# Optimization experiments

Measured on AMD Instinct MI355X. Metric: run time of the kernel, lower is better.

The kernel has to match this reference:

```python
import jax, jax.numpy as jnp
import numpy as np

N = 50000   # nodes
E = 800000  # edges
F = 128     # feature dim per layer
BN_EPS = 1e-5


def setup_inputs() -> dict:
    key = jax.random.key(0)
    ks = jax.random.split(key, 4)
    x = jax.random.normal(ks[0], (N, F), dtype=jnp.float32)
    edge_index = jax.random.randint(ks[1], (2, E), 0, N, dtype=jnp.int64)
    scale = 1.0 / np.sqrt(F)
    W1 = jax.random.normal(ks[2], (F, F), dtype=jnp.float32) * scale
    W2 = jax.random.normal(ks[3], (F, F), dtype=jnp.float32) * scale
    zeros = jnp.zeros((F,), dtype=jnp.float32)
    ones = jnp.ones((F,), dtype=jnp.float32)
    prelu = jnp.full((1,), 0.25, dtype=jnp.float32)
    return {
        "x": x, "edge_index": edge_index,
        "W1": W1, "b1": zeros, "g1": ones, "be1": zeros, "a1": prelu,
        "W2": W2, "b2": zeros, "g2": ones, "be2": zeros, "a2": prelu,
    }


def _gcn_norm(edge_index):
    # PyG GCNConv: add self-loops, symmetric normalization D^-1/2 A D^-1/2
    src, dst = edge_index[0], edge_index[1]
    loop = jnp.arange(N, dtype=src.dtype)
    src_a = jnp.concatenate([src, loop])  # [E+N]
    dst_a = jnp.concatenate([dst, loop])
    w = jnp.ones((E + N,), dtype=jnp.float32)
    deg = jax.ops.segment_sum(w, dst_a, num_segments=N)
    dinv = jnp.where(deg > 0, jax.lax.rsqrt(jnp.maximum(deg, 1.0)), 0.0)
    norm = dinv[src_a] * w * dinv[dst_a]  # [E+N]
    return src_a, dst_a, norm


def _layer(x, src_a, dst_a, norm, W, b, g, be, a):
    h = x @ W                                    # [N,F] dense transform
    msg = h[src_a] * norm[:, None]               # gather [E+N,F]
    agg = jax.ops.segment_sum(msg, dst_a, num_segments=N) + b  # scatter-add
    # BatchNorm1d (training mode: biased batch statistics over nodes)
    mu = jnp.mean(agg, axis=0)
    var = jnp.mean(jnp.square(agg - mu), axis=0)
    xh = (agg - mu) * jax.lax.rsqrt(var + BN_EPS) * g + be
    # PReLU (single shared weight)
    return jnp.where(xh >= 0, xh, a * xh)


def reference(x, edge_index, W1, b1, g1, be1, a1, W2, b2, g2, be2, a2):
    src_a, dst_a, norm = _gcn_norm(edge_index)
    x = _layer(x, src_a, dst_a, norm, W1, b1, g1, be1, a1)
    x = _layer(x, src_a, dst_a, norm, W2, b2, g2, be2, a2)
    return x
```

## Files before the change

### kernel.cpp

```cpp
#include <hip/hip_runtime.h>

#define FD 128
#define BN_EPS 1e-5f
#define BSH 8
#define CAP 6144
#define BE 8192
#define NGB 2048
#define NRB 64

typedef short s8v __attribute__((ext_vector_type(8)));
typedef float f4v __attribute__((ext_vector_type(4)));

__device__ __forceinline__ unsigned short f2bf(float f) {
    unsigned u = __float_as_uint(f);
    u += 0x7fff + ((u >> 16) & 1);
    return (unsigned short)(u >> 16);
}
__device__ __forceinline__ unsigned pack2(float a, float b) {
    return (unsigned)f2bf(a) | ((unsigned)f2bf(b) << 16);
}
__device__ __forceinline__ float bf_lo(unsigned int u) {
    return __uint_as_float(u << 16);
}
__device__ __forceinline__ float bf_hi(unsigned int u) {
    return __uint_as_float(u & 0xffff0000u);
}
__device__ __forceinline__ float bfu(unsigned short s) {
    return __uint_as_float(((unsigned)s) << 16);
}

__device__ __forceinline__ int edge_get(const void* ei, int is64, size_t idx) {
    return is64 ? (int)((const long long*)ei)[idx] : ((const int*)ei)[idx];
}

__global__ __launch_bounds__(256) void partition_kernel(const void* ei,
                                                        int* __restrict__ gcur,
                                                        unsigned* __restrict__ slab, int E) {
    __shared__ int any;
    __shared__ int hist[256];
    __shared__ int base[256];
    __shared__ int cur[256];
    int t = threadIdx.x;
    if (t == 0) any = 0;
    hist[t] = 0;
    __syncthreads();
    {
        const int* e32 = (const int*)ei;
        int limit = 2 * E < 4096 ? 2 * E : 4096;
        int found = 0;
        for (int i = t * 2 + 1; i < limit; i += 512)
            if (e32[i] != 0) { found = 1; break; }
        if (found) atomicOr(&any, 1);
    }
    __syncthreads();
    int is64 = any ? 0 : 1;
    int e0 = blockIdx.x * BE;
    int cnt = E - e0; if (cnt > BE) cnt = BE;
    for (int i = t; i < cnt; i += 256) {
        int d = edge_get(ei, is64, (size_t)E + e0 + i);
        atomicAdd(&hist[d >> BSH], 1);
    }
    __syncthreads();
    base[t] = hist[t] ? atomicAdd(&gcur[t], hist[t]) : 0;
    cur[t] = 0;
    __syncthreads();
    for (int i = t; i < cnt; i += 256) {
        int s = edge_get(ei, is64, e0 + i);
        int d = edge_get(ei, is64, (size_t)E + e0 + i);
        int b = d >> BSH;
        int r = atomicAdd(&cur[b], 1);
        int pos = base[b] + r;
        if (pos < CAP)
            slab[(size_t)b * CAP + pos] = (unsigned)s | ((unsigned)(d & 255) << 24);
    }
}

__global__ __launch_bounds__(256) void bucket_csr_kernel(const unsigned* __restrict__ slab,
                                                         const int* __restrict__ gcur,
                                                         int* __restrict__ colslab,
                                                         uint4* __restrict__ nodemeta,
                                                         float* __restrict__ dinv, int n) {
    __shared__ int hist[256];
    __shared__ int loc[256];
    __shared__ int cur[256];
    __shared__ int tmp[256];
    int b = blockIdx.x, t = threadIdx.x;
    hist[t] = 0;
    __syncthreads();
    int cnt = gcur[b]; if (cnt > CAP) cnt = CAP;
    const unsigned* sl = slab + (size_t)b * CAP;
    for (int i = t; i < cnt; i += 256)
        atomicAdd(&hist[sl[i] >> 24], 1);
    __syncthreads();
    int v = hist[t];
    tmp[t] = v;
    __syncthreads();
    for (int off = 1; off < 256; off <<= 1) {
        int x = (t >= off) ? tmp[t - off] : 0;
        __syncthreads();
        tmp[t] += x;
        __syncthreads();
    }
    int start_loc = tmp[t] - v;
    loc[t] = start_loc;
    cur[t] = 0;
    int node = (b << BSH) + t;
    if (node < n) {
        float dv = rsqrtf(1.0f + (float)v);
        dinv[node] = dv;
        nodemeta[node] = make_uint4((unsigned)(b * CAP + start_loc), (unsigned)v,
                                    __float_as_uint(dv), 0u);
    }
    __syncthreads();
    for (int i = t; i < cnt; i += 256) {
        unsigned e = sl[i];
        int dl = e >> 24;
        int r = atomicAdd(&cur[dl], 1);
        colslab[(size_t)b * CAP + loc[dl] + r] = (int)(e & 0xFFFFFF);
    }
}

__global__ __launch_bounds__(256) void wprep_kernel(const float* __restrict__ W1,
                                                    const float* __restrict__ W2,
                                                    unsigned short* __restrict__ Wf1,
                                                    unsigned short* __restrict__ Wf2) {
    int blk = blockIdx.x;
    const float* W = (blk < 64) ? W1 : W2;
    unsigned short* Wf = (blk < 64) ? Wf1 : Wf2;
    int idx = (blk & 63) * 256 + threadIdx.x;
    int j = idx & 7, lane = (idx >> 3) & 63, ct = (idx >> 9) & 7, kt = idx >> 12;
    int k = kt * 32 + (lane >> 4) * 8 + j;
    int c = ct * 16 + (lane & 15);
    Wf[idx] = f2bf(W[k * FD + c]);
}

template<int MODE>
__global__ __launch_bounds__(256) void gemm_mfma_kernel(const void* __restrict__ Ain,
                                                        const unsigned short* __restrict__ Wfrag,
                                                        const float* __restrict__ dinv,
                                                        const float4* __restrict__ scsh,
                                                        const float* __restrict__ aP,
                                                        unsigned short* __restrict__ C,
                                                        int n) {
    int wave = threadIdx.x >> 6, lane = threadIdx.x & 63;
    int rbase = blockIdx.x * 64 + wave * 16;
    int lrow = rbase + (lane & 15);
    int kg = lane >> 4;
    bool rok = lrow < n;
    float alpha = MODE ? aP[0] : 0.f;

    f4v acc[8];
#pragma unroll
    for (int i = 0; i < 8; ++i) acc[i] = (f4v){0.f, 0.f, 0.f, 0.f};

    const s8v* wf = (const s8v*)Wfrag;

#pragma unroll
    for (int kt = 0; kt < 4; ++kt) {
        s8v afr = (s8v){0, 0, 0, 0, 0, 0, 0, 0};
        if (rok) {
            float4 u0, u1;
            if (MODE) {
                const unsigned short* A = (const unsigned short*)Ain;
                s8v raw = *(const s8v*)(A + (size_t)lrow * FD + kt * 32 + kg * 8);
                u0.x = bfu((unsigned short)raw[0]); u0.y = bfu((unsigned short)raw[1]);
                u0.z = bfu((unsigned short)raw[2]); u0.w = bfu((unsigned short)raw[3]);
                u1.x = bfu((unsigned short)raw[4]); u1.y = bfu((unsigned short)raw[5]);
                u1.z = bfu((unsigned short)raw[6]); u1.w = bfu((unsigned short)raw[7]);
                int c4 = kt * 8 + kg * 2;
                float4 sc0 = scsh[c4],      sh0 = scsh[32 + c4];
                float4 sc1 = scsh[c4 + 1],  sh1 = scsh[32 + c4 + 1];
                u0.x = u0.x * sc0.x + sh0.x; u0.y = u0.y * sc0.y + sh0.y;
                u0.z = u0.z * sc0.z + sh0.z; u0.w = u0.w * sc0.w + sh0.w;
                u1.x = u1.x * sc1.x + sh1.x; u1.y = u1.y * sc1.y + sh1.y;
                u1.z = u1.z * sc1.z + sh1.z; u1.w = u1.w * sc1.w + sh1.w;
                u0.x = u0.x >= 0.f ? u0.x : alpha * u0.x;
                u0.y = u0.y >= 0.f ? u0.y : alpha * u0.y;
                u0.z = u0.z >= 0.f ? u0.z : alpha * u0.z;
                u0.w = u0.w >= 0.f ? u0.w : alpha * u0.w;
                u1.x = u1.x >= 0.f ? u1.x : alpha * u1.x;
                u1.y = u1.y >= 0.f ? u1.y : alpha * u1.y;
                u1.z = u1.z >= 0.f ? u1.z : alpha * u1.z;
                u1.w = u1.w >= 0.f ? u1.w : alpha * u1.w;
            } else {
                const float* A = (const float*)Ain;
                const float* p = A + (size_t)lrow * FD + kt * 32 + kg * 8;
                u0 = *(const float4*)p;
                u1 = *(const float4*)(p + 4);
            }
            afr[0] = (short)f2bf(u0.x); afr[1] = (short)f2bf(u0.y);
            afr[2] = (short)f2bf(u0.z); afr[3] = (short)f2bf(u0.w);
            afr[4] = (short)f2bf(u1.x); afr[5] = (short)f2bf(u1.y);
            afr[6] = (short)f2bf(u1.z); afr[7] = (short)f2bf(u1.w);
        }
#pragma unroll
        for (int ct = 0; ct < 8; ++ct) {
            s8v bfr = wf[(kt * 8 + ct) * 64 + lane];
            acc[ct] = __builtin_amdgcn_mfma_f32_16x16x32_bf16(afr, bfr, acc[ct], 0, 0, 0);
        }
    }

    int col0 = lane & 15;
#pragma unroll
    for (int r = 0; r < 4; ++r) {
        int row = rbase + kg * 4 + r;
        if (row < n) {
            float dv = dinv[row];
            unsigned short* crow = C + (size_t)row * FD;
#pragma unroll
            for (int ct = 0; ct < 8; ++ct)
                crow[ct * 16 + col0] = f2bf(acc[ct][r] * dv);
        }
    }
}

__global__ __launch_bounds__(256) void gather_stats_kernel(const uint2* __restrict__ hs2,
                                                           const uint4* __restrict__ nodemeta,
                                                           const int* __restrict__ col,
                                                           const float* __restrict__ b,
                                                           uint2* __restrict__ aggb,
                                                           float4* __restrict__ partial,
                                                           int n) {
    __shared__ float4 redS[256];
    __shared__ float4 redQ[256];
    int tid = threadIdx.x;
    int hid = blockIdx.x * 8 + (tid >> 5);
    int q = tid & 31;
    float4 bb = ((const float4*)b)[q];

    float4 ssum = {0.f, 0.f, 0.f, 0.f};
    float4 ssq  = {0.f, 0.f, 0.f, 0.f};

    for (int wid = hid; wid < n; wid += NGB * 8) {
        uint4 m = nodemeta[wid];
        int i0 = (int)m.x, cnt = (int)m.y;
        float dv = __uint_as_float(m.z);
        uint2 u = hs2[(size_t)wid * 32 + q];
        float ax = bf_lo(u.x), ay = bf_hi(u.x), az = bf_lo(u.y), aw = bf_hi(u.y);
        int j = 0;
        for (; j + 4 <= cnt; j += 4) {
            int s0 = col[i0 + j], s1 = col[i0 + j + 1];
            int s2 = col[i0 + j + 2], s3 = col[i0 + j + 3];
            uint2 u0 = hs2[(size_t)s0 * 32 + q];
            uint2 u1 = hs2[(size_t)s1 * 32 + q];
            uint2 u2 = hs2[(size_t)s2 * 32 + q];
            uint2 u3 = hs2[(size_t)s3 * 32 + q];
            ax += bf_lo(u0.x) + bf_lo(u1.x) + bf_lo(u2.x) + bf_lo(u3.x);
            ay += bf_hi(u0.x) + bf_hi(u1.x) + bf_hi(u2.x) + bf_hi(u3.x);
            az += bf_lo(u0.y) + bf_lo(u1.y) + bf_lo(u2.y) + bf_lo(u3.y);
            aw += bf_hi(u0.y) + bf_hi(u1.y) + bf_hi(u2.y) + bf_hi(u3.y);
        }
        for (; j < cnt; ++j) {
            int s = col[i0 + j];
            uint2 uu = hs2[(size_t)s * 32 + q];
            ax += bf_lo(uu.x); ay += bf_hi(uu.x); az += bf_lo(uu.y); aw += bf_hi(uu.y);
        }
        float4 o;
        o.x = dv * ax + bb.x; o.y = dv * ay + bb.y;
        o.z = dv * az + bb.z; o.w = dv * aw + bb.w;
        uint2 w;
        w.x = pack2(o.x, o.y);
        w.y = pack2(o.z, o.w);
        aggb[(size_t)wid * 32 + q] = w;
        ssum.x += o.x; ssum.y += o.y; ssum.z += o.z; ssum.w += o.w;
        ssq.x += o.x * o.x; ssq.y += o.y * o.y;
        ssq.z += o.z * o.z; ssq.w += o.w * o.w;
    }
    redS[tid] = ssum;
    redQ[tid] = ssq;
    __syncthreads();
    if (tid < 128) {
        redS[tid].x += redS[tid+128].x; redS[tid].y += redS[tid+128].y;
        redS[tid].z += redS[tid+128].z; redS[tid].w += redS[tid+128].w;
        redQ[tid].x += redQ[tid+128].x; redQ[tid].y += redQ[tid+128].y;
        redQ[tid].z += redQ[tid+128].z; redQ[tid].w += redQ[tid+128].w;
    }
    __syncthreads();
    if (tid < 64) {
        redS[tid].x += redS[tid+64].x; redS[tid].y += redS[tid+64].y;
        redS[tid].z += redS[tid+64].z; redS[tid].w += redS[tid+64].w;
        redQ[tid].x += redQ[tid+64].x; redQ[tid].y += redQ[tid+64].y;
        redQ[tid].z += redQ[tid+64].z; redQ[tid].w += redQ[tid+64].w;
    }
    __syncthreads();
    if (tid < 32) {
        float4 s = redS[tid], s2 = redS[tid + 32];
        float4 qq = redQ[tid], q2 = redQ[tid + 32];
        s.x += s2.x; s.y += s2.y; s.z += s2.z; s.w += s2.w;
        qq.x += q2.x; qq.y += q2.y; qq.z += q2.z; qq.w += q2.w;
        partial[(size_t)blockIdx.x * 64 + tid] = s;
        partial[(size_t)blockIdx.x * 64 + 32 + tid] = qq;
    }
}

__global__ __launch_bounds__(256) void reduce_partial_kernel(const float4* __restrict__ partial,
                                                             float4* __restrict__ partial2) {
    __shared__ float4 red[256];
    int t = threadIdx.x;
    int e = t & 63;
    int sr = t >> 6;
    int r0 = blockIdx.x * 32;
    float4 acc = {0.f, 0.f, 0.f, 0.f};
    for (int r = sr; r < 32; r += 4) {
        float4 v = partial[(size_t)(r0 + r) * 64 + e];
        acc.x += v.x; acc.y += v.y; acc.z += v.z; acc.w += v.w;
    }
    red[t] = acc;
    __syncthreads();
    if (sr < 2) {
        float4 o = red[t + 128];
        red[t].x += o.x; red[t].y += o.y; red[t].z += o.z; red[t].w += o.w;
    }
    __syncthreads();
    if (sr == 0) {
        float4 o = red[t + 64];
        float4 s = red[t];
        s.x += o.x; s.y += o.y; s.z += o.z; s.w += o.w;
        partial2[(size_t)blockIdx.x * 64 + e] = s;
    }
}

__global__ __launch_bounds__(1024) void bn_finalize_kernel(const float4* __restrict__ partial2,
                                                           const float* __restrict__ g,
                                                           const float* __restrict__ be,
                                                           float4* __restrict__ scsh,
                                                           float invn) {
    __shared__ float4 red[1024];
    int t = threadIdx.x;
    int e = t & 63;
    int rg = t >> 6;
    float4 acc = {0.f, 0.f, 0.f, 0.f};
    for (int r = rg; r < NRB; r += 16) {
        float4 v = partial2[(size_t)r * 64 + e];
        acc.x += v.x; acc.y += v.y; acc.z += v.z; acc.w += v.w;
    }
    red[t] = acc;
    __syncthreads();
#pragma unroll
    for (int s = 8; s >= 1; s >>= 1) {
        if (rg < s) {
            float4 o = red[t + s * 64];
            red[t].x += o.x; red[t].y += o.y; red[t].z += o.z; red[t].w += o.w;
        }
        __syncthreads();
    }
    if (t < 32) {
        float4 s = red[t];
        float4 qq = red[32 + t];
        float4 gg = ((const float4*)g)[t];
        float4 bbe = ((const float4*)be)[t];
        float4 mu, var, sc, sh;
        mu.x = s.x * invn; mu.y = s.y * invn; mu.z = s.z * invn; mu.w = s.w * invn;
        var.x = qq.x * invn - mu.x * mu.x; var.y = qq.y * invn - mu.y * mu.y;
        var.z = qq.z * invn - mu.z * mu.z; var.w = qq.w * invn - mu.w * mu.w;
        sc.x = gg.x * rsqrtf(var.x + BN_EPS); sc.y = gg.y * rsqrtf(var.y + BN_EPS);
        sc.z = gg.z * rsqrtf(var.z + BN_EPS); sc.w = gg.w * rsqrtf(var.w + BN_EPS);
        sh.x = bbe.x - mu.x * sc.x; sh.y = bbe.y - mu.y * sc.y;
        sh.z = bbe.z - mu.z * sc.z; sh.w = bbe.w - mu.w * sc.w;
        scsh[t] = sc;
        scsh[32 + t] = sh;
    }
}

__global__ __launch_bounds__(256) void bn_apply_kernel(const uint2* __restrict__ aggb,
                                                       const float4* __restrict__ scsh,
                                                       const float* __restrict__ aP,
                                                       float4* __restrict__ out, int n) {
    int t = blockIdx.x * 256 + threadIdx.x;
    if (t >= n * 32) return;
    int c4 = t & 31;
    float alpha = aP[0];
    uint2 u = aggb[t];
    float4 v;
    v.x = bf_lo(u.x); v.y = bf_hi(u.x); v.z = bf_lo(u.y); v.w = bf_hi(u.y);
    float4 sc = scsh[c4];
    float4 sh = scsh[32 + c4];
    float4 y;
    y.x = v.x * sc.x + sh.x; y.y = v.y * sc.y + sh.y;
    y.z = v.z * sc.z + sh.z; y.w = v.w * sc.w + sh.w;
    y.x = y.x >= 0.f ? y.x : alpha * y.x;
    y.y = y.y >= 0.f ? y.y : alpha * y.y;
    y.z = y.z >= 0.f ? y.z : alpha * y.z;
    y.w = y.w >= 0.f ? y.w : alpha * y.w;
    out[t] = y;
}


extern "C" void kernel_launch(void* const* d_in, const int* in_sizes, int n_in,
                              void* d_out, int out_size, void* d_ws, size_t ws_size,
                              hipStream_t stream) {
    const float* x  = (const float*)d_in[0];
    const void*  ei = d_in[1];
    const float* W1 = (const float*)d_in[2];
    const float* b1 = (const float*)d_in[3];
    const float* g1 = (const float*)d_in[4];
    const float* be1= (const float*)d_in[5];
    const float* a1 = (const float*)d_in[6];
    const float* W2 = (const float*)d_in[7];
    const float* b2 = (const float*)d_in[8];
    const float* g2 = (const float*)d_in[9];
    const float* be2= (const float*)d_in[10];
    const float* a2 = (const float*)d_in[11];

    int N = in_sizes[0] / FD;
    int E = in_sizes[1] / 2;
    float* out = (float*)d_out;

    int nbuck = (N + (1 << BSH) - 1) >> BSH;

    char* ws = (char*)d_ws;
    size_t off = 0;
    auto alloc = [&](size_t bytes) {
        void* p = ws + off;
        off += (bytes + 255) & ~(size_t)255;
        return p;
    };
    float* dinv    = (float*)alloc((size_t)N * 4);
    int*   gcur    = (int*)alloc(256 * 4);
    uint4* nodemeta= (uint4*)alloc((size_t)N * 16);
    unsigned* slab = (unsigned*)alloc((size_t)nbuck * CAP * 4);
    int*   colslab = (int*)alloc((size_t)nbuck * CAP * 4);
    unsigned short* wf1 = (unsigned short*)alloc((size_t)FD * FD * 2);
    unsigned short* wf2 = (unsigned short*)alloc((size_t)FD * FD * 2);
    unsigned short* hs  = (unsigned short*)alloc((size_t)N * FD * 2);
    uint2* aggb    = (uint2*)alloc((size_t)N * FD * 2);
    float4* partial= (float4*)alloc((size_t)NGB * 64 * 16);
    float4* partial2=(float4*)alloc((size_t)NRB * 64 * 16);
    float4* scsh   = (float4*)alloc(64 * 16);
    (void)ws_size; (void)n_in; (void)out_size;

    hipMemsetAsync(gcur, 0, 256 * 4, stream);

    partition_kernel<<<(E + BE - 1) / BE, 256, 0, stream>>>(ei, gcur, slab, E);
    bucket_csr_kernel<<<nbuck, 256, 0, stream>>>(slab, gcur, colslab, nodemeta, dinv, N);

    wprep_kernel<<<128, 256, 0, stream>>>(W1, W2, wf1, wf2);

    int gemm_blocks = (N + 63) / 64;
    int nt = N * 32;
    float invn = 1.0f / (float)N;

    gemm_mfma_kernel<0><<<gemm_blocks, 256, 0, stream>>>(x, wf1, dinv, nullptr, nullptr,
                                                         hs, N);
    gather_stats_kernel<<<NGB, 256, 0, stream>>>((const uint2*)hs, nodemeta, colslab,
                                                 b1, aggb, partial, N);
    reduce_partial_kernel<<<NRB, 256, 0, stream>>>(partial, partial2);
    bn_finalize_kernel<<<1, 1024, 0, stream>>>(partial2, g1, be1, scsh, invn);

    gemm_mfma_kernel<1><<<gemm_blocks, 256, 0, stream>>>(aggb, wf2, dinv,
                                                         scsh, a1, hs, N);
    gather_stats_kernel<<<NGB, 256, 0, stream>>>((const uint2*)hs, nodemeta, colslab,
                                                 b2, aggb, partial, N);
    reduce_partial_kernel<<<NRB, 256, 0, stream>>>(partial, partial2);
    bn_finalize_kernel<<<1, 1024, 0, stream>>>(partial2, g2, be2, scsh, invn);
    bn_apply_kernel<<<(nt + 255) / 256, 256, 0, stream>>>(aggb, scsh, a2, (float4*)out, N);
}
```

Before: 165.2 us.

## Widen gather loads, fuse BN reduce and finalize, fold counter reset

The gather kernel now has each half-warp read 16-byte bf16 rows. Two lane groups split a node's edge list, and their partial sums are combined with a cross-lane shuffle. Stats partials are written as flat floats. The two-stage BN reduction and the finalize kernel become one kernel, where the last block to finish (found with an atomic counter) computes scale and shift. The memset for the partition counter is folded into the weight-prep kernel, which now launches first. Together these aim to cut kernel launches and issue wider, fewer memory requests in the edge gather. The cost is threadfence and atomic ordering, plus shuffles and lane divergence in the gather.

Result: slower. 181.5 us (+9.9%).

```diff
diff --git a/kernel.cpp b/kernel.cpp
--- a/kernel.cpp
+++ b/kernel.cpp
@@ -31,6 +31,22 @@
 
 __device__ __forceinline__ int edge_get(const void* ei, int is64, size_t idx) {
     return is64 ? (int)((const long long*)ei)[idx] : ((const int*)ei)[idx];
+}
+
+__global__ __launch_bounds__(256) void wprep_kernel(const float* __restrict__ W1,
+                                                    const float* __restrict__ W2,
+                                                    unsigned short* __restrict__ Wf1,
+                                                    unsigned short* __restrict__ Wf2,
+                                                    int* __restrict__ gcur) {
+    int blk = blockIdx.x;
+    if (blk == 0 && threadIdx.x < 258) gcur[threadIdx.x] = 0;
+    const float* W = (blk < 64) ? W1 : W2;
+    unsigned short* Wf = (blk < 64) ? Wf1 : Wf2;
+    int idx = (blk & 63) * 256 + threadIdx.x;
+    int j = idx & 7, lane = (idx >> 3) & 63, ct = (idx >> 9) & 7, kt = idx >> 12;
+    int k = kt * 32 + (lane >> 4) * 8 + j;
+    int c = ct * 16 + (lane & 15);
+    Wf[idx] = f2bf(W[k * FD + c]);
 }
 
 __global__ __launch_bounds__(256) void partition_kernel(const void* ei,
@@ -118,20 +134,6 @@
         int r = atomicAdd(&cur[dl], 1);
         colslab[(size_t)b * CAP + loc[dl] + r] = (int)(e & 0xFFFFFF);
     }
-}
-
-__global__ __launch_bounds__(256) void wprep_kernel(const float* __restrict__ W1,
-                                                    const float* __restrict__ W2,
-                                                    unsigned short* __restrict__ Wf1,
-                                                    unsigned short* __restrict__ Wf2) {
-    int blk = blockIdx.x;
-    const float* W = (blk < 64) ? W1 : W2;
-    unsigned short* Wf = (blk < 64) ? Wf1 : Wf2;
-    int idx = (blk & 63) * 256 + threadIdx.x;
-    int j = idx & 7, lane = (idx >> 3) & 63, ct = (idx >> 9) & 7, kt = idx >> 12;
-    int k = kt * 32 + (lane >> 4) * 8 + j;
-    int c = ct * 16 + (lane & 15);
-    Wf[idx] = f2bf(W[k * FD + c]);
 }
 
 template<int MODE>
@@ -214,97 +216,148 @@
     }
 }
 
-__global__ __launch_bounds__(256) void gather_stats_kernel(const uint2* __restrict__ hs2,
+__global__ __launch_bounds__(256) void gather_stats_kernel(const uint4* __restrict__ hs4,
                                                            const uint4* __restrict__ nodemeta,
                                                            const int* __restrict__ col,
                                                            const float* __restrict__ b,
-                                                           uint2* __restrict__ aggb,
-                                                           float4* __restrict__ partial,
+                                                           uint4* __restrict__ aggb4,
+                                                           float* __restrict__ partialf,
+                                                           int* __restrict__ done,
                                                            int n) {
-    __shared__ float4 redS[256];
-    __shared__ float4 redQ[256];
+    __shared__ float redS[1024];
+    __shared__ float redQ[1024];
     int tid = threadIdx.x;
-    int hid = blockIdx.x * 8 + (tid >> 5);
-    int q = tid & 31;
-    float4 bb = ((const float4*)b)[q];
-
-    float4 ssum = {0.f, 0.f, 0.f, 0.f};
-    float4 ssq  = {0.f, 0.f, 0.f, 0.f};
+    if (blockIdx.x == 0 && tid == 0) done[0] = 0;
+    int half = tid >> 5;
+    int g = (tid >> 4) & 1;
+    int c = tid & 15;
+    int hid = blockIdx.x * 8 + half;
+
+    float bb[8];
+    {
+        const float4* b4 = (const float4*)b;
+        float4 blo = b4[c * 2], bhi = b4[c * 2 + 1];
+        bb[0] = blo.x; bb[1] = blo.y; bb[2] = blo.z; bb[3] = blo.w;
+        bb[4] = bhi.x; bb[5] = bhi.y; bb[6] = bhi.z; bb[7] = bhi.w;
+    }
+    float ss[8], sq[8];
+#pragma unroll
+    for (int k = 0; k < 8; ++k) { ss[k] = 0.f; sq[k] = 0.f; }
 
     for (int wid = hid; wid < n; wid += NGB * 8) {
         uint4 m = nodemeta[wid];
         int i0 = (int)m.x, cnt = (int)m.y;
         float dv = __uint_as_float(m.z);
-        uint2 u = hs2[(size_t)wid * 32 + q];
-        float ax = bf_lo(u.x), ay = bf_hi(u.x), az = bf_lo(u.y), aw = bf_hi(u.y);
-        int j = 0;
-        for (; j + 4 <= cnt; j += 4) {
-            int s0 = col[i0 + j], s1 = col[i0 + j + 1];
-            int s2 = col[i0 + j + 2], s3 = col[i0 + j + 3];
-            uint2 u0 = hs2[(size_t)s0 * 32 + q];
-            uint2 u1 = hs2[(size_t)s1 * 32 + q];
-            uint2 u2 = hs2[(size_t)s2 * 32 + q];
-            uint2 u3 = hs2[(size_t)s3 * 32 + q];
-            ax += bf_lo(u0.x) + bf_lo(u1.x) + bf_lo(u2.x) + bf_lo(u3.x);
-            ay += bf_hi(u0.x) + bf_hi(u1.x) + bf_hi(u2.x) + bf_hi(u3.x);
-            az += bf_lo(u0.y) + bf_lo(u1.y) + bf_lo(u2.y) + bf_lo(u3.y);
-            aw += bf_hi(u0.y) + bf_hi(u1.y) + bf_hi(u2.y) + bf_hi(u3.y);
-        }
-        for (; j < cnt; ++j) {
+        float a[8];
+#pragma unroll
+        for (int k = 0; k < 8; ++k) a[k] = 0.f;
+        if (g == 0) {
+            uint4 u = hs4[(size_t)wid * 16 + c];
+            a[0] += bf_lo(u.x); a[1] += bf_hi(u.x); a[2] += bf_lo(u.y); a[3] += bf_hi(u.y);
+            a[4] += bf_lo(u.z); a[5] += bf_hi(u.z); a[6] += bf_lo(u.w); a[7] += bf_hi(u.w);
+        }
+        int j = g;
+        for (; j + 6 < cnt; j += 8) {
+            int s0 = col[i0 + j],     s1 = col[i0 + j + 2];
+            int s2 = col[i0 + j + 4], s3 = col[i0 + j + 6];
+            uint4 u0 = hs4[(size_t)s0 * 16 + c];
+            uint4 u1 = hs4[(size_t)s1 * 16 + c];
+            uint4 u2 = hs4[(size_t)s2 * 16 + c];
+            uint4 u3 = hs4[(size_t)s3 * 16 + c];
+            a[0] += bf_lo(u0.x) + bf_lo(u1.x) + bf_lo(u2.x) + bf_lo(u3.x);
+            a[1] += bf_hi(u0.x) + bf_hi(u1.x) + bf_hi(u2.x) + bf_hi(u3.x);
+            a[2] += bf_lo(u0.y) + bf_lo(u1.y) + bf_lo(u2.y) + bf_lo(u3.y);
+            a[3] += bf_hi(u0.y) + bf_hi(u1.y) + bf_hi(u2.y) + bf_hi(u3.y);
+            a[4] += bf_lo(u0.z) + bf_lo(u1.z) + bf_lo(u2.z) + bf_lo(u3.z);
+            a[5] += bf_hi(u0.z) + bf_hi(u1.z) + bf_hi(u2.z) + bf_hi(u3.z);
+            a[6] += bf_lo(u0.w) + bf_lo(u1.w) + bf_lo(u2.w) + bf_lo(u3.w);
+            a[7] += bf_hi(u0.w) + bf_hi(u1.w) + bf_hi(u2.w) + bf_hi(u3.w);
+        }
+        for (; j < cnt; j += 2) {
             int s = col[i0 + j];
-            uint2 uu = hs2[(size_t)s * 32 + q];
-            ax += bf_lo(uu.x); ay += bf_hi(uu.x); az += bf_lo(uu.y); aw += bf_hi(uu.y);
-        }
-        float4 o;
-        o.x = dv * ax + bb.x; o.y = dv * ay + bb.y;
-        o.z = dv * az + bb.z; o.w = dv * aw + bb.w;
-        uint2 w;
-        w.x = pack2(o.x, o.y);
-        w.y = pack2(o.z, o.w);
-        aggb[(size_t)wid * 32 + q] = w;
-        ssum.x += o.x; ssum.y += o.y; ssum.z += o.z; ssum.w += o.w;
-        ssq.x += o.x * o.x; ssq.y += o.y * o.y;
-        ssq.z += o.z * o.z; ssq.w += o.w * o.w;
-    }
-    redS[tid] = ssum;
-    redQ[tid] = ssq;
+            uint4 u = hs4[(size_t)s * 16 + c];
+            a[0] += bf_lo(u.x); a[1] += bf_hi(u.x); a[2] += bf_lo(u.y); a[3] += bf_hi(u.y);
+            a[4] += bf_lo(u.z); a[5] += bf_hi(u.z); a[6] += bf_lo(u.w); a[7] += bf_hi(u.w);
+        }
+#pragma unroll
+        for (int k = 0; k < 8; ++k) a[k] += __shfl_xor(a[k], 16);
+        if (g == 0) {
+            float o[8];
+#pragma unroll
+            for (int k = 0; k < 8; ++k) o[k] = dv * a[k] + bb[k];
+            uint4 w;
+            w.x = pack2(o[0], o[1]); w.y = pack2(o[2], o[3]);
+            w.z = pack2(o[4], o[5]); w.w = pack2(o[6], o[7]);
+            aggb4[(size_t)wid * 16 + c] = w;
+#pragma unroll
+            for (int k = 0; k < 8; ++k) { ss[k] += o[k]; sq[k] += o[k] * o[k]; }
+        }
+    }
+    if (g == 0) {
+#pragma unroll
+        for (int k = 0; k < 8; ++k) {
+            redS[half * 128 + c * 8 + k] = ss[k];
+            redQ[half * 128 + c * 8 + k] = sq[k];
+        }
+    }
     __syncthreads();
     if (tid < 128) {
-        redS[tid].x += redS[tid+128].x; redS[tid].y += redS[tid+128].y;
-        redS[tid].z += redS[tid+128].z; redS[tid].w += redS[tid+128].w;
-        redQ[tid].x += redQ[tid+128].x; redQ[tid].y += redQ[tid+128].y;
-        redQ[tid].z += redQ[tid+128].z; redQ[tid].w += redQ[tid+128].w;
-    }
-    __syncthreads();
-    if (tid < 64) {
-        redS[tid].x += redS[tid+64].x; redS[tid].y += redS[tid+64].y;
-        redS[tid].z += redS[tid+64].z; redS[tid].w += redS[tid+64].w;
-        redQ[tid].x += redQ[tid+64].x; redQ[tid].y += redQ[tid+64].y;
-        redQ[tid].z += redQ[tid+64].z; redQ[tid].w += redQ[tid+64].w;
-    }
-    __syncthreads();
-    if (tid < 32) {
-        float4 s = redS[tid], s2 = redS[tid + 32];
-        float4 qq = redQ[tid], q2 = redQ[tid + 32];
-        s.x += s2.x; s.y += s2.y; s.z += s2.z; s.w += s2.w;
-        qq.x += q2.x; qq.y += q2.y; qq.z += q2.z; qq.w += q2.w;
-        partial[(size_t)blockIdx.x * 64 + tid] = s;
-        partial[(size_t)blockIdx.x * 64 + 32 + tid] = qq;
-    }
-}
-
-__global__ __launch_bounds__(256) void reduce_partial_kernel(const float4* __restrict__ partial,
-                                                             float4* __restrict__ partial2) {
+        float s = 0.f, q = 0.f;
+#pragma unroll
+        for (int h = 0; h < 8; ++h) {
+            s += redS[h * 128 + tid];
+            q += redQ[h * 128 + tid];
+        }
+        partialf[(size_t)blockIdx.x * 256 + tid] = s;
+        partialf[(size_t)blockIdx.x * 256 + 128 + tid] = q;
+    }
+}
+
+__global__ __launch_bounds__(256) void reduce_finalize_kernel(const float4* __restrict__ partial,
+                                                              float4* __restrict__ partial2,
+                                                              int* __restrict__ done,
+                                                              const float* __restrict__ g,
+                                                              const float* __restrict__ be,
+                                                              float4* __restrict__ scsh,
+                                                              float invn) {
     __shared__ float4 red[256];
+    __shared__ int isLast;
     int t = threadIdx.x;
     int e = t & 63;
     int sr = t >> 6;
-    int r0 = blockIdx.x * 32;
+    {
+        int r0 = blockIdx.x * 32;
+        float4 acc = {0.f, 0.f, 0.f, 0.f};
+        for (int r = sr; r < 32; r += 4) {
+            float4 v = partial[(size_t)(r0 + r) * 64 + e];
+            acc.x += v.x; acc.y += v.y; acc.z += v.z; acc.w += v.w;
+        }
+        red[t] = acc;
+        __syncthreads();
+        if (sr < 2) {
+            float4 o = red[t + 128];
+            red[t].x += o.x; red[t].y += o.y; red[t].z += o.z; red[t].w += o.w;
+        }
+        __syncthreads();
+        if (sr == 0) {
+            float4 o = red[t + 64];
+            float4 s = red[t];
+            s.x += o.x; s.y += o.y; s.z += o.z; s.w += o.w;
+            partial2[(size_t)blockIdx.x * 64 + e] = s;
+        }
+    }
+    __syncthreads();
+    __threadfence();
+    if (t == 0) isLast = (atomicAdd(done, 1) == (int)gridDim.x - 1);
+    __syncthreads();
+    if (!isLast) return;
+    __threadfence();
     float4 acc = {0.f, 0.f, 0.f, 0.f};
-    for (int r = sr; r < 32; r += 4) {
-        float4 v = partial[(size_t)(r0 + r) * 64 + e];
+    for (int r = sr; r < NRB; r += 4) {
+        float4 v = partial2[(size_t)r * 64 + e];
         acc.x += v.x; acc.y += v.y; acc.z += v.z; acc.w += v.w;
     }
+    __syncthreads();
     red[t] = acc;
     __syncthreads();
     if (sr < 2) {
@@ -314,36 +367,9 @@
     __syncthreads();
     if (sr == 0) {
         float4 o = red[t + 64];
-        float4 s = red[t];
-        s.x += o.x; s.y += o.y; s.z += o.z; s.w += o.w;
-        partial2[(size_t)blockIdx.x * 64 + e] = s;
-    }
-}
-
-__global__ __launch_bounds__(1024) void bn_finalize_kernel(const float4* __restrict__ partial2,
-                                                           const float* __restrict__ g,
-                                                           const float* __restrict__ be,
-                                                           float4* __restrict__ scsh,
-                                                           float invn) {
-    __shared__ float4 red[1024];
-    int t = threadIdx.x;
-    int e = t & 63;
-    int rg = t >> 6;
-    float4 acc = {0.f, 0.f, 0.f, 0.f};
-    for (int r = rg; r < NRB; r += 16) {
-        float4 v = partial2[(size_t)r * 64 + e];
-        acc.x += v.x; acc.y += v.y; acc.z += v.z; acc.w += v.w;
-    }
-    red[t] = acc;
-    __syncthreads();
-#pragma unroll
-    for (int s = 8; s >= 1; s >>= 1) {
-        if (rg < s) {
-            float4 o = red[t + s * 64];
-            red[t].x += o.x; red[t].y += o.y; red[t].z += o.z; red[t].w += o.w;
-        }
-        __syncthreads();
-    }
+        red[t].x += o.x; red[t].y += o.y; red[t].z += o.z; red[t].w += o.w;
+    }
+    __syncthreads();
     if (t < 32) {
         float4 s = red[t];
         float4 qq = red[32 + t];
@@ -416,25 +442,24 @@
         return p;
     };
     float* dinv    = (float*)alloc((size_t)N * 4);
-    int*   gcur    = (int*)alloc(256 * 4);
+    int*   gcur    = (int*)alloc(260 * 4);
+    int*   done    = gcur + 256;
     uint4* nodemeta= (uint4*)alloc((size_t)N * 16);
     unsigned* slab = (unsigned*)alloc((size_t)nbuck * CAP * 4);
     int*   colslab = (int*)alloc((size_t)nbuck * CAP * 4);
     unsigned short* wf1 = (unsigned short*)alloc((size_t)FD * FD * 2);
     unsigned short* wf2 = (unsigned short*)alloc((size_t)FD * FD * 2);
     unsigned short* hs  = (unsigned short*)alloc((size_t)N * FD * 2);
-    uint2* aggb    = (uint2*)alloc((size_t)N * FD * 2);
-    float4* partial= (float4*)alloc((size_t)NGB * 64 * 16);
+    uint4* aggb    = (uint4*)alloc((size_t)N * FD * 2);
+    float* partialf= (float*)alloc((size_t)NGB * 256 * 4);
     float4* partial2=(float4*)alloc((size_t)NRB * 64 * 16);
     float4* scsh   = (float4*)alloc(64 * 16);
     (void)ws_size; (void)n_in; (void)out_size;
 
-    hipMemsetAsync(gcur, 0, 256 * 4, stream);
+    wprep_kernel<<<128, 256, 0, stream>>>(W1, W2, wf1, wf2, gcur);
 
     partition_kernel<<<(E + BE - 1) / BE, 256, 0, stream>>>(ei, gcur, slab, E);
     bucket_csr_kernel<<<nbuck, 256, 0, stream>>>(slab, gcur, colslab, nodemeta, dinv, N);
-
-    wprep_kernel<<<128, 256, 0, stream>>>(W1, W2, wf1, wf2);
 
     int gemm_blocks = (N + 63) / 64;
     int nt = N * 32;
@@ -442,16 +467,17 @@
 
     gemm_mfma_kernel<0><<<gemm_blocks, 256, 0, stream>>>(x, wf1, dinv, nullptr, nullptr,
                                                          hs, N);
-    gather_stats_kernel<<<NGB, 256, 0, stream>>>((const uint2*)hs, nodemeta, colslab,
-                                                 b1, aggb, partial, N);
-    reduce_partial_kernel<<<NRB, 256, 0, stream>>>(partial, partial2);
-    bn_finalize_kernel<<<1, 1024, 0, stream>>>(partial2, g1, be1, scsh, invn);
+    gather_stats_kernel<<<NGB, 256, 0, stream>>>((const uint4*)hs, nodemeta, colslab,
+                                                 b1, aggb, partialf, done, N);
+    reduce_finalize_kernel<<<NRB, 256, 0, stream>>>((const float4*)partialf, partial2,
+                                                    done, g1, be1, scsh, invn);
 
     gemm_mfma_kernel<1><<<gemm_blocks, 256, 0, stream>>>(aggb, wf2, dinv,
                                                          scsh, a1, hs, N);
-    gather_stats_kernel<<<NGB, 256, 0, stream>>>((const uint2*)hs, nodemeta, colslab,
-                                                 b2, aggb, partial, N);
-    reduce_partial_kernel<<<NRB, 256, 0, stream>>>(partial, partial2);
-    bn_finalize_kernel<<<1, 1024, 0, stream>>>(partial2, g2, be2, scsh, invn);
-    bn_apply_kernel<<<(nt + 255) / 256, 256, 0, stream>>>(aggb, scsh, a2, (float4*)out, N);
-}
+    gather_stats_kernel<<<NGB, 256, 0, stream>>>((const uint4*)hs, nodemeta, colslab,
+                                                 b2, aggb, partialf, done, N);
+    reduce_finalize_kernel<<<NRB, 256, 0, stream>>>((const float4*)partialf, partial2,
+                                                    done, g2, be2, scsh, invn);
+    bn_apply_kernel<<<(nt + 255) / 256, 256, 0, stream>>>((const uint2*)aggb, scsh, a2,
+                                                          (float4*)out, N);
+}
```
